# Kernel tuning notes

Hardware: AMD Instinct MI355X
Metric: run time of the kernel (lower is better)

The kernel has to match this reference:

```python
import jax, jax.numpy as jnp
import numpy as np

B, T, S, E, H = 2, 1024, 1024, 1024, 16
D = E // H  # head_dim = 64
SCALING = D ** -0.5


def setup_inputs() -> dict:
    key = jax.random.key(0)
    ks = jax.random.split(key, 14)
    inv = 1.0 / np.sqrt(E)
    inp = {
        "query": jax.random.normal(ks[0], (B, T, E), jnp.float32),
        "key": jax.random.normal(ks[1], (B, S, E), jnp.float32),
        "value": jax.random.normal(ks[2], (B, S, E), jnp.float32),
        "key_padding_mask": jax.random.bernoulli(ks[3], 0.1, (B, S)),
        "attn_bias": jax.random.normal(ks[4], (B * H, T, S), jnp.float32),
        "Wq": jax.random.uniform(ks[5], (E, E), jnp.float32, -inv, inv),
        "bq": jax.random.uniform(ks[6], (E,), jnp.float32, -inv, inv),
        "Wk": jax.random.uniform(ks[7], (E, E), jnp.float32, -inv, inv),
        "bk": jax.random.uniform(ks[8], (E,), jnp.float32, -inv, inv),
        "Wv": jax.random.uniform(ks[9], (E, E), jnp.float32, -inv, inv),
        "bv": jax.random.uniform(ks[10], (E,), jnp.float32, -inv, inv),
        "Wo": jax.random.uniform(ks[11], (E, E), jnp.float32, -inv, inv),
        "bo": jax.random.uniform(ks[12], (E,), jnp.float32, -inv, inv),
    }
    return inp


def reference(query, key, value, key_padding_mask, attn_bias,
              Wq, bq, Wk, bk, Wv, bv, Wo, bo):
    # Projections (torch Linear: x @ W.T + b)
    q = query @ Wq.T + bq  # [B, T, E]
    k = key @ Wk.T + bk    # [B, S, E]
    v = value @ Wv.T + bv  # [B, S, E]
    # Split heads -> [B, H, L, D]
    q = q.reshape(B, T, H, D).transpose(0, 2, 1, 3) * SCALING
    k = k.reshape(B, S, H, D).transpose(0, 2, 1, 3)
    v = v.reshape(B, S, H, D).transpose(0, 2, 1, 3)
    # Scores [B, H, T, S]
    attn_weights = jnp.einsum('bhtd,bhsd->bhts', q, k)
    # key_padding_mask: True means masked -> -inf (applied BEFORE bias add)
    attn_weights = jnp.where(key_padding_mask[:, None, None, :], -jnp.inf, attn_weights)
    # softmax_dropout with additive bias (eval mode: dropout is identity)
    attn_weights = attn_weights + attn_bias.reshape(B, H, T, S)
    attn = jax.nn.softmax(attn_weights, axis=-1)
    o = jnp.einsum('bhts,bhsd->bhtd', attn, v)  # [B, H, T, D]
    o = o.transpose(0, 2, 1, 3).reshape(B, T, E)
    return o @ Wo.T + bo
```

## Files before the change

### kernel.cpp

```cpp
#include <hip/hip_runtime.h>
#include <math.h>
#include <stdint.h>

#define B_ 2
#define T_ 1024
#define S_ 1024
#define E_ 1024
#define H_ 16
#define SCALING_ 0.125f

typedef short bf16x8 __attribute__((ext_vector_type(8)));
typedef float f32x4 __attribute__((ext_vector_type(4)));
typedef unsigned short us8 __attribute__((ext_vector_type(8)));
typedef unsigned short ush;

__device__ __forceinline__ ush f2bf(float x) {
    unsigned int u = __float_as_uint(x);
    return (ush)((u + 0x7fffu + ((u >> 16) & 1u)) >> 16);
}
__device__ __forceinline__ float bf2f(ush h) {
    return __uint_as_float(((unsigned int)h) << 16);
}
__device__ __forceinline__ void split_bf(float x, ush& hh, ush& ll) {
    hh = f2bf(x);
    ll = f2bf(x - bf2f(hh));
}
__device__ __forceinline__ void gl_lds16(const void* g, void* l) {
    __builtin_amdgcn_global_load_lds(
        (const __attribute__((address_space(1))) unsigned int*)g,
        (__attribute__((address_space(3))) unsigned int*)l, 16, 0, 0);
}
template <int CTRL>
__device__ __forceinline__ float dpp_ror(float x) {
    int v = __builtin_amdgcn_update_dpp(0, __float_as_int(x), CTRL, 0xf, 0xf, true);
    return __int_as_float(v);
}
#define FENCE() asm volatile("" ::: "memory")
#define BARRIER() do { FENCE(); __builtin_amdgcn_s_barrier(); FENCE(); } while (0)

__global__ void mask_detect_kernel(const unsigned int* __restrict__ p,
                                   int* __restrict__ mode_out) {
    __shared__ int gt1_s, oddnz_s;
    if (threadIdx.x == 0) { gt1_s = 0; oddnz_s = 0; }
    __syncthreads();
    int gt1 = 0;
    for (int i = threadIdx.x; i < 512; i += 256)
        if (p[i] > 1u) gt1 = 1;
    if (gt1) atomicOr(&gt1_s, 1);
    __syncthreads();
    if (gt1_s == 0) {
        int oddnz = 0;
        for (int i = threadIdx.x; i < 2048; i += 256)
            if ((i & 1) && p[i] != 0u) oddnz = 1;
        if (oddnz) atomicOr(&oddnz_s, 1);
    }
    __syncthreads();
    if (threadIdx.x == 0)
        *mode_out = gt1_s ? 1 : (oddnz_s ? 0 : 2);
}

__global__ void mask_norm_kernel(const void* __restrict__ p,
                                 const int* __restrict__ mode_p,
                                 int* __restrict__ mout) {
    int i = blockIdx.x * 256 + threadIdx.x;
    int mode = *mode_p;
    int v;
    if (mode == 1)      v = (int)((const unsigned char*)p)[i];
    else if (mode == 2) v = ((const int*)p)[2 * i];
    else                v = ((const int*)p)[i];
    mout[i] = v;
}

__global__ __launch_bounds__(256) void conv_split7_kernel(
    const float* __restrict__ Wq, const float* __restrict__ Wk,
    const float* __restrict__ Wv, const float* __restrict__ Wo,
    const float* __restrict__ xq, const float* __restrict__ xk,
    const float* __restrict__ xv,
    ush* __restrict__ Wqh, ush* __restrict__ Wql,
    ush* __restrict__ Wkh, ush* __restrict__ Wkl,
    ush* __restrict__ Wvh, ush* __restrict__ Wvl,
    ush* __restrict__ Woh, ush* __restrict__ Wol,
    ush* __restrict__ xqh, ush* __restrict__ xql,
    ush* __restrict__ xkh, ush* __restrict__ xkl,
    ush* __restrict__ xvh, ush* __restrict__ xvl) {
    int bid = blockIdx.x;
    const float* src; ush* dh; ush* dl; int lb;
    if (bid < 2048) {
        int w = bid >> 9; lb = bid & 511;
        if (w == 0)      { src = Wq; dh = Wqh; dl = Wql; }
        else if (w == 1) { src = Wk; dh = Wkh; dl = Wkl; }
        else if (w == 2) { src = Wv; dh = Wvh; dl = Wvl; }
        else             { src = Wo; dh = Woh; dl = Wol; }
    } else {
        int a = (bid - 2048) >> 10; lb = (bid - 2048) & 1023;
        if (a == 0)      { src = xq; dh = xqh; dl = xql; }
        else if (a == 1) { src = xk; dh = xkh; dl = xkl; }
        else             { src = xv; dh = xvh; dl = xvl; }
    }
    int i = (lb * 256 + threadIdx.x) * 8;
    float4 a4 = *(const float4*)&src[i];
    float4 b4 = *(const float4*)&src[i + 4];
    float v[8] = {a4.x, a4.y, a4.z, a4.w, b4.x, b4.y, b4.z, b4.w};
    us8 vh, vl;
#pragma unroll
    for (int j = 0; j < 8; j++) {
        ush hh, ll;
        split_bf(v[j], hh, ll);
        vh[j] = hh; vl[j] = ll;
    }
    *(us8*)&dh[i] = vh;
    *(us8*)&dl[i] = vl;
}

template <int N, int K, int ROWBIAS, int SPLITOUT>
__device__ __forceinline__ void gemm_body3(
    int bid,
    const ush* __restrict__ Ahg, const ush* __restrict__ Alg,
    const ush* __restrict__ Bhg, const ush* __restrict__ Blg,
    const float* __restrict__ bias,
    ush* __restrict__ outh, ush* __restrict__ outl,
    float* __restrict__ outf, float alpha, ush* lds) {
    const int tid = threadIdx.x;
    const int lane = tid & 63;
    const int wave = tid >> 6;
    const int wm = wave >> 1, wn = wave & 1;
    const int bn = bid % (N / 64);
    const int bm = bid / (N / 64);
    const int m0 = bm * 64, n0 = bn * 64;
    constexpr int NT = K / 32;
    const int row = tid >> 2, oct = tid & 3;
    const int oct2 = oct ^ ((row >> 1) & 3);

    f32x4 acc[2][2];
#pragma unroll
    for (int i = 0; i < 2; i++)
#pragma unroll
        for (int j = 0; j < 2; j++) acc[i][j] = (f32x4){0.f, 0.f, 0.f, 0.f};

    auto stage = [&](int k0, ush* buf) {
        size_t ga = (size_t)(m0 + row) * K + k0 + oct2 * 8;
        gl_lds16(&Ahg[ga], &buf[tid * 8]);
        gl_lds16(&Alg[ga], &buf[2048 + tid * 8]);
        size_t gb = (size_t)(n0 + row) * K + k0 + oct2 * 8;
        gl_lds16(&Bhg[gb], &buf[4096 + tid * 8]);
        gl_lds16(&Blg[gb], &buf[6144 + tid * 8]);
    };

    ush* p0 = lds;
    ush* p1 = lds + 8192;
    ush* p2 = lds + 16384;
    stage(0, p0);
    stage(32, p1);

    for (int t = 0; t < NT; t++) {
        if (t + 1 < NT) asm volatile("s_waitcnt vmcnt(4)" ::: "memory");
        else            asm volatile("s_waitcnt vmcnt(0)" ::: "memory");
        BARRIER();
        if (t + 2 < NT) stage((t + 2) * 32, p2);

        bf16x8 afr[2][2], bfr[2][2];
#pragma unroll
        for (int nj = 0; nj < 2; nj++) {
            int rowB = wn * 32 + nj * 16 + (lane & 15);
            int ch = (lane >> 4) ^ ((rowB >> 1) & 3);
            bfr[nj][0] = *(const bf16x8*)&p0[4096 + rowB * 32 + ch * 8];
            bfr[nj][1] = *(const bf16x8*)&p0[6144 + rowB * 32 + ch * 8];
        }
#pragma unroll
        for (int mi = 0; mi < 2; mi++) {
            int rowA = wm * 32 + mi * 16 + (lane & 15);
            int ch = (lane >> 4) ^ ((rowA >> 1) & 3);
            afr[mi][0] = *(const bf16x8*)&p0[rowA * 32 + ch * 8];
            afr[mi][1] = *(const bf16x8*)&p0[2048 + rowA * 32 + ch * 8];
        }
        __builtin_amdgcn_s_setprio(1);
#pragma unroll
        for (int mi = 0; mi < 2; mi++)
#pragma unroll
            for (int nj = 0; nj < 2; nj++) {
                acc[mi][nj] = __builtin_amdgcn_mfma_f32_16x16x32_bf16(afr[mi][0], bfr[nj][0], acc[mi][nj], 0, 0, 0);
                acc[mi][nj] = __builtin_amdgcn_mfma_f32_16x16x32_bf16(afr[mi][1], bfr[nj][0], acc[mi][nj], 0, 0, 0);
                acc[mi][nj] = __builtin_amdgcn_mfma_f32_16x16x32_bf16(afr[mi][0], bfr[nj][1], acc[mi][nj], 0, 0, 0);
            }
        __builtin_amdgcn_s_setprio(0);

        ush* tmp = p0; p0 = p1; p1 = p2; p2 = tmp;
    }

    float bcol[2];
    if (!ROWBIAS) {
#pragma unroll
        for (int nj = 0; nj < 2; nj++)
            bcol[nj] = bias[n0 + wn * 32 + nj * 16 + (lane & 15)];
    }
#pragma unroll
    for (int mi = 0; mi < 2; mi++) {
#pragma unroll
        for (int r = 0; r < 4; r++) {
            int orow = m0 + wm * 32 + mi * 16 + (lane >> 4) * 4 + r;
            float brow = ROWBIAS ? bias[orow] : 0.f;
#pragma unroll
            for (int nj = 0; nj < 2; nj++) {
                int col = n0 + wn * 32 + nj * 16 + (lane & 15);
                float v = alpha * (acc[mi][nj][r] + (ROWBIAS ? brow : bcol[nj]));
                if (SPLITOUT) {
                    ush hh, ll;
                    split_bf(v, hh, ll);
                    outh[(size_t)orow * N + col] = hh;
                    outl[(size_t)orow * N + col] = ll;
                } else {
                    outf[(size_t)orow * N + col] = v;
                }
            }
        }
    }
}

__global__ __launch_bounds__(256) void proj_fused_kernel(
    const ush* __restrict__ xqh, const ush* __restrict__ xql,
    const ush* __restrict__ xkh, const ush* __restrict__ xkl,
    const ush* __restrict__ xvh, const ush* __restrict__ xvl,
    const ush* __restrict__ Wqh, const ush* __restrict__ Wql,
    const ush* __restrict__ Wkh, const ush* __restrict__ Wkl,
    const ush* __restrict__ Wvh, const ush* __restrict__ Wvl,
    const float* __restrict__ bq, const float* __restrict__ bk,
    const float* __restrict__ bv_,
    ush* __restrict__ qh, ush* __restrict__ ql,
    ush* __restrict__ kh, ush* __restrict__ kl,
    ush* __restrict__ vth, ush* __restrict__ vtl) {
    __shared__ __align__(16) ush lds[3 * 8192];
    int op = blockIdx.x / 512;
    int bid = blockIdx.x % 512;
    if (op == 0)
        gemm_body3<1024, 1024, 0, 1>(bid, xqh, xql, Wqh, Wql, bq,
                                     qh, ql, nullptr, SCALING_, lds);
    else if (op == 1)
        gemm_body3<1024, 1024, 0, 1>(bid, xkh, xkl, Wkh, Wkl, bk,
                                     kh, kl, nullptr, 1.f, lds);
    else
        gemm_body3<2048, 1024, 1, 1>(bid, Wvh, Wvl, xvh, xvl, bv_,
                                     vth, vtl, nullptr, 1.f, lds);
}

__global__ __launch_bounds__(256) void gemm_out_kernel(
    const ush* __restrict__ oh, const ush* __restrict__ ol,
    const ush* __restrict__ Woh, const ush* __restrict__ Wol,
    const float* __restrict__ bo, float* __restrict__ out) {
    __shared__ __align__(16) ush lds[3 * 8192];
    gemm_body3<1024, 1024, 0, 0>(blockIdx.x, oh, ol, Woh, Wol, bo,
                                 nullptr, nullptr, out, 1.f, lds);
}

__global__ __launch_bounds__(256) void flash_kernel(
    const ush* __restrict__ qh, const ush* __restrict__ ql,
    const ush* __restrict__ kh, const ush* __restrict__ kl,
    const ush* __restrict__ vth, const ush* __restrict__ vtl,
    const float* __restrict__ bias, const int* __restrict__ mask,
    ush* __restrict__ oh, ush* __restrict__ ol) {
    __shared__ __align__(16) ush Ksh[2][4096], Ksl[2][4096];
    __shared__ __align__(16) ush Vsh[4096], Vsl[4096];
    __shared__ __align__(16) float BPb[2][4096];

    const int tid = threadIdx.x;
    const int lane = tid & 63;
    const int wave = tid >> 6;
    const int bh = blockIdx.x >> 4;
    const int tt = blockIdx.x & 15;
    const int b = bh >> 4, h = bh & 15;
    const int t0 = tt * 64;
    const int srow = tid >> 3;
    const int soct = tid & 7;

#pragma unroll
    for (int p = 0; p < 2; p++) {
        int row = p * 32 + srow;
        int oc2 = soct ^ (row & 7);
        size_t g = (size_t)(b * T_ + t0 + row) * E_ + h * 64 + oc2 * 8;
        gl_lds16(&qh[g], &Ksh[0][row * 64 + soct * 8]);
        gl_lds16(&ql[g], &Ksl[0][row * 64 + soct * 8]);
    }
    asm volatile("s_waitcnt vmcnt(0)" ::: "memory");
    __syncthreads();
    bf16x8 qfh[2], qfl[2];
    {
        int row = wave * 16 + (lane & 15);
#pragma unroll
        for (int kk = 0; kk < 2; kk++) {
            int ch = (kk * 4 + (lane >> 4)) ^ (row & 7);
            qfh[kk] = *(const bf16x8*)&Ksh[0][row * 64 + ch * 8];
            qfl[kk] = *(const bf16x8*)&Ksl[0][row * 64 + ch * 8];
        }
    }
    __syncthreads();

    float mrow[4] = {-INFINITY, -INFINITY, -INFINITY, -INFINITY};
    float lrow[4] = {0.f, 0.f, 0.f, 0.f};
    f32x4 oacc[4];
#pragma unroll
    for (int dj = 0; dj < 4; dj++) oacc[dj] = (f32x4){0.f, 0.f, 0.f, 0.f};

    auto stage_k = [&](int ti, int c) {
#pragma unroll
        for (int p = 0; p < 2; p++) {
            int row = p * 32 + srow;
            int oc2 = soct ^ (row & 7);
            size_t gk = (size_t)(b * S_ + ti * 64 + row) * E_ + h * 64 + oc2 * 8;
            gl_lds16(&kh[gk], &Ksh[c][row * 64 + soct * 8]);
            gl_lds16(&kl[gk], &Ksl[c][row * 64 + soct * 8]);
        }
    };
    auto stage_v = [&](int ti) {
#pragma unroll
        for (int p = 0; p < 2; p++) {
            int row = p * 32 + srow;
            int oc2 = soct ^ (row & 7);
            size_t gv = (size_t)(h * 64 + row) * (B_ * S_) + b * S_ + ti * 64 + oc2 * 8;
            gl_lds16(&vth[gv], &Vsh[row * 64 + soct * 8]);
            gl_lds16(&vtl[gv], &Vsl[row * 64 + soct * 8]);
        }
    };
    auto stage_bias = [&](int ti, int reg) {
#pragma unroll
        for (int p = 0; p < 4; p++) {
            int row = p * 16 + (tid >> 4);
            int slot = tid & 15;
            int sslot = slot ^ (((row >> 2) & 1) << 2);
            const float* src = bias + ((size_t)bh * T_ + t0 + row) * S_ +
                               ti * 64 + sslot * 4;
            gl_lds16(src, &BPb[reg][(p * 256 + tid) * 4]);
        }
    };

    int mk[4];
    stage_k(0, 0);
    stage_v(0);
    stage_bias(0, 0);
#pragma unroll
    for (int nj = 0; nj < 4; nj++)
        mk[nj] = mask[b * S_ + nj * 16 + (lane & 15)];
    asm volatile("s_waitcnt vmcnt(0)" ::: "memory");
    __syncthreads();

    for (int t = 0; t < 16; t++) {
        const int cur = t & 1;

        if (t < 15) {
            stage_k(t + 1, cur ^ 1);
            stage_bias(t + 1, cur ^ 1);
        }

        f32x4 sc[4];
#pragma unroll
        for (int nj = 0; nj < 4; nj++) sc[nj] = (f32x4){0.f, 0.f, 0.f, 0.f};
        __builtin_amdgcn_s_setprio(1);
#pragma unroll
        for (int kk = 0; kk < 2; kk++) {
#pragma unroll
            for (int nj = 0; nj < 4; nj++) {
                int row = nj * 16 + (lane & 15);
                int ch = (kk * 4 + (lane >> 4)) ^ (row & 7);
                bf16x8 kfh = *(const bf16x8*)&Ksh[cur][row * 64 + ch * 8];
                bf16x8 kfl = *(const bf16x8*)&Ksl[cur][row * 64 + ch * 8];
                sc[nj] = __builtin_amdgcn_mfma_f32_16x16x32_bf16(qfh[kk], kfh, sc[nj], 0, 0, 0);
                sc[nj] = __builtin_amdgcn_mfma_f32_16x16x32_bf16(qfl[kk], kfh, sc[nj], 0, 0, 0);
                sc[nj] = __builtin_amdgcn_mfma_f32_16x16x32_bf16(qfh[kk], kfl, sc[nj], 0, 0, 0);
            }
        }
        __builtin_amdgcn_s_setprio(0);

        {
            const float* bp = &BPb[cur][wave * 1024];
#pragma unroll
            for (int r = 0; r < 4; r++) {
                int tl = (lane >> 4) * 4 + r;
                int sx = ((tl >> 2) & 1) << 4;
#pragma unroll
                for (int nj = 0; nj < 4; nj++) {
                    int s = (nj * 16 + (lane & 15)) ^ sx;
                    float bvv = bp[tl * 64 + s];
                    float v = mk[nj] ? -INFINITY : sc[nj][r];
                    sc[nj][r] = v + bvv;
                }
            }
        }
        if (t < 15) {
            const int s0n = (t + 1) * 64;
#pragma unroll
            for (int nj = 0; nj < 4; nj++)
                mk[nj] = mask[b * S_ + s0n + nj * 16 + (lane & 15)];
        }

        ush phv[4][4], plv[4][4];
#pragma unroll
        for (int r = 0; r < 4; r++) {
            float mx = fmaxf(fmaxf(sc[0][r], sc[1][r]), fmaxf(sc[2][r], sc[3][r]));
            mx = fmaxf(mx, dpp_ror<0x121>(mx));
            mx = fmaxf(mx, dpp_ror<0x122>(mx));
            mx = fmaxf(mx, dpp_ror<0x124>(mx));
            mx = fmaxf(mx, dpp_ror<0x128>(mx));
            float mnew = fmaxf(mrow[r], mx);
            float esc = __expf(mrow[r] - mnew);
            float ps = 0.f;
#pragma unroll
            for (int nj = 0; nj < 4; nj++) {
                float p = __expf(sc[nj][r] - mnew);
                ps += p;
                split_bf(p, phv[nj][r], plv[nj][r]);
            }
            ps += dpp_ror<0x121>(ps);
            ps += dpp_ror<0x122>(ps);
            ps += dpp_ror<0x124>(ps);
            ps += dpp_ror<0x128>(ps);
            lrow[r] = lrow[r] * esc + ps;
            mrow[r] = mnew;
#pragma unroll
            for (int dj = 0; dj < 4; dj++) oacc[dj][r] *= esc;
        }

        ush* Pw = (ush*)&BPb[cur][wave * 1024];
#pragma unroll
        for (int r = 0; r < 4; r++) {
            int tq = (lane >> 4) * 4 + r;
            int f = (((tq >> 2) & 3) << 1) | (tq & 1);
#pragma unroll
            for (int nj = 0; nj < 4; nj++) {
                int s = nj * 16 + (lane & 15);
                int idx = tq * 64 + (((s >> 3) ^ f) * 8) + (s & 7);
                Pw[idx] = phv[nj][r];
                Pw[1024 + idx] = plv[nj][r];
            }
        }
        bf16x8 pah[2], pal[2];
        {
            int tq = lane & 15;
            int f = (((tq >> 2) & 3) << 1) | (tq & 1);
#pragma unroll
            for (int kk = 0; kk < 2; kk++) {
                int ch = (kk * 4 + (lane >> 4)) ^ f;
                pah[kk] = *(const bf16x8*)&Pw[tq * 64 + ch * 8];
                pal[kk] = *(const bf16x8*)&Pw[1024 + tq * 64 + ch * 8];
            }
        }

        if (t < 15) asm volatile("s_waitcnt vmcnt(8)" ::: "memory");
        else        asm volatile("s_waitcnt vmcnt(0)" ::: "memory");

        __builtin_amdgcn_s_setprio(1);
#pragma unroll
        for (int dj = 0; dj < 4; dj++) {
            int row = dj * 16 + (lane & 15);
#pragma unroll
            for (int kk = 0; kk < 2; kk++) {
                int ch = (kk * 4 + (lane >> 4)) ^ (row & 7);
                bf16x8 vfh = *(const bf16x8*)&Vsh[row * 64 + ch * 8];
                bf16x8 vfl = *(const bf16x8*)&Vsl[row * 64 + ch * 8];
                oacc[dj] = __builtin_amdgcn_mfma_f32_16x16x32_bf16(pah[kk], vfh, oacc[dj], 0, 0, 0);
                oacc[dj] = __builtin_amdgcn_mfma_f32_16x16x32_bf16(pal[kk], vfh, oacc[dj], 0, 0, 0);
                oacc[dj] = __builtin_amdgcn_mfma_f32_16x16x32_bf16(pah[kk], vfl, oacc[dj], 0, 0, 0);
            }
        }
        __builtin_amdgcn_s_setprio(0);

        asm volatile("s_waitcnt vmcnt(0)" ::: "memory");
        BARRIER();
        if (t < 15) stage_v(t + 1);
    }

#pragma unroll
    for (int r = 0; r < 4; r++) {
        float inv = 1.f / lrow[r];
        int t = t0 + wave * 16 + (lane >> 4) * 4 + r;
#pragma unroll
        for (int dj = 0; dj < 4; dj++) {
            float v = oacc[dj][r] * inv;
            ush hh, ll;
            split_bf(v, hh, ll);
            size_t g = (size_t)(b * T_ + t) * E_ + h * 64 + dj * 16 + (lane & 15);
            oh[g] = hh;
            ol[g] = ll;
        }
    }
}

extern "C" void kernel_launch(void* const* d_in, const int* in_sizes, int n_in,
                              void* d_out, int out_size, void* d_ws,
                              size_t ws_size, hipStream_t stream) {
    const float* query = (const float*)d_in[0];
    const float* key   = (const float*)d_in[1];
    const float* value = (const float*)d_in[2];
    const void*  kpm   = d_in[3];
    const float* attn_bias = (const float*)d_in[4];
    const float* Wq = (const float*)d_in[5];
    const float* bq = (const float*)d_in[6];
    const float* Wk = (const float*)d_in[7];
    const float* bk = (const float*)d_in[8];
    const float* Wv = (const float*)d_in[9];
    const float* bv = (const float*)d_in[10];
    const float* Wo = (const float*)d_in[11];
    const float* bo = (const float*)d_in[12];
    float* out = (float*)d_out;

    char* ws = (char*)d_ws;
    const size_t MB = 1024 * 1024;
    ush* Wqh = (ush*)(ws + 0 * MB);
    ush* Wql = (ush*)(ws + 2 * MB);
    ush* Wkh = (ush*)(ws + 4 * MB);
    ush* Wkl = (ush*)(ws + 6 * MB);
    ush* Wvh = (ush*)(ws + 8 * MB);
    ush* Wvl = (ush*)(ws + 10 * MB);
    ush* Woh = (ush*)(ws + 12 * MB);
    ush* Wol = (ush*)(ws + 14 * MB);
    ush* qh  = (ush*)(ws + 16 * MB);
    ush* ql  = (ush*)(ws + 20 * MB);
    ush* kh  = (ush*)(ws + 24 * MB);
    ush* kl  = (ush*)(ws + 28 * MB);
    ush* vth = (ush*)(ws + 32 * MB);
    ush* vtl = (ush*)(ws + 36 * MB);
    ush* xqh = (ush*)(ws + 40 * MB);
    ush* xql = (ush*)(ws + 44 * MB);
    ush* xkh = (ush*)(ws + 48 * MB);
    ush* xkl = (ush*)(ws + 52 * MB);
    ush* xvh = (ush*)(ws + 56 * MB);
    ush* xvl = (ush*)(ws + 60 * MB);
    ush* oh  = (ush*)(ws + 40 * MB);
    ush* ol  = (ush*)(ws + 44 * MB);
    int* masknorm = (int*)(ws + 64 * MB);
    int* mode = masknorm + 2048;

    conv_split7_kernel<<<5120, 256, 0, stream>>>(
        Wq, Wk, Wv, Wo, query, key, value,
        Wqh, Wql, Wkh, Wkl, Wvh, Wvl, Woh, Wol,
        xqh, xql, xkh, xkl, xvh, xvl);
    mask_detect_kernel<<<1, 256, 0, stream>>>((const unsigned int*)kpm, mode);
    mask_norm_kernel<<<8, 256, 0, stream>>>(kpm, mode, masknorm);

    proj_fused_kernel<<<1536, 256, 0, stream>>>(
        xqh, xql, xkh, xkl, xvh, xvl,
        Wqh, Wql, Wkh, Wkl, Wvh, Wvl, bq, bk, bv,
        qh, ql, kh, kl, vth, vtl);

    flash_kernel<<<512, 256, 0, stream>>>(qh, ql, kh, kl, vth, vtl, attn_bias,
                                          masknorm, oh, ol);

    gemm_out_kernel<<<512, 256, 0, stream>>>(oh, ol, Woh, Wol, bo, out);
}
```

Baseline: 344.9 us.

## Load attention bias directly into registers and reuse K buffer for P staging

Attention bias is no longer staged through a shared-memory double buffer. Each lane now loads its bias values and mask straight from global memory into ping-pong register arrays, one tile ahead. The P tile staging moves into the current K buffer slot, which frees the bias LDS space and should raise occupancy. The vmcnt waits and barriers are reordered to fit the new load counts. The trade-off is more registers, scalar (non-vectorized) global bias loads, and fragile hand-counted vmcnt values.

```diff
diff --git a/kernel.cpp b/kernel.cpp
--- a/kernel.cpp
+++ b/kernel.cpp
@@ -259,14 +259,13 @@
     ush* __restrict__ oh, ush* __restrict__ ol) {
     __shared__ __align__(16) ush Ksh[2][4096], Ksl[2][4096];
     __shared__ __align__(16) ush Vsh[4096], Vsl[4096];
-    __shared__ __align__(16) float BPb[2][4096];
 
     const int tid = threadIdx.x;
     const int lane = tid & 63;
     const int wave = tid >> 6;
-    const int bh = blockIdx.x >> 4;
+    const int bhid = blockIdx.x >> 4;
     const int tt = blockIdx.x & 15;
-    const int b = bh >> 4, h = bh & 15;
+    const int b = bhid >> 4, h = bhid & 15;
     const int t0 = tt * 64;
     const int srow = tid >> 3;
     const int soct = tid & 7;
@@ -299,6 +298,8 @@
 #pragma unroll
     for (int dj = 0; dj < 4; dj++) oacc[dj] = (f32x4){0.f, 0.f, 0.f, 0.f};
 
+    const size_t bias0 = ((size_t)bhid * T_ + t0 + wave * 16) * S_;
+
     auto stage_k = [&](int ti, int c) {
 #pragma unroll
         for (int p = 0; p < 2; p++) {
@@ -319,34 +320,39 @@
             gl_lds16(&vtl[gv], &Vsl[row * 64 + soct * 8]);
         }
     };
-    auto stage_bias = [&](int ti, int reg) {
-#pragma unroll
-        for (int p = 0; p < 4; p++) {
-            int row = p * 16 + (tid >> 4);
-            int slot = tid & 15;
-            int sslot = slot ^ (((row >> 2) & 1) << 2);
-            const float* src = bias + ((size_t)bh * T_ + t0 + row) * S_ +
-                               ti * 64 + sslot * 4;
-            gl_lds16(src, &BPb[reg][(p * 256 + tid) * 4]);
-        }
-    };
-
-    int mk[4];
+
+    float bvA[4][4], bvB[4][4];
+    int mkA[4], mkB[4];
+
     stage_k(0, 0);
     stage_v(0);
-    stage_bias(0, 0);
-#pragma unroll
-    for (int nj = 0; nj < 4; nj++)
-        mk[nj] = mask[b * S_ + nj * 16 + (lane & 15)];
+    FENCE();
+#pragma unroll
+    for (int nj = 0; nj < 4; nj++) {
+        int s = nj * 16 + (lane & 15);
+        mkA[nj] = mask[b * S_ + s];
+#pragma unroll
+        for (int r = 0; r < 4; r++)
+            bvA[nj][r] = bias[bias0 + (size_t)((lane >> 4) * 4 + r) * S_ + s];
+    }
     asm volatile("s_waitcnt vmcnt(0)" ::: "memory");
     __syncthreads();
 
-    for (int t = 0; t < 16; t++) {
-        const int cur = t & 1;
-
+    auto iter = [&](int t, int cur, float (&bvU)[4][4], float (&bvL)[4][4],
+                    int (&mkU)[4], int (&mkL)[4]) {
         if (t < 15) {
             stage_k(t + 1, cur ^ 1);
-            stage_bias(t + 1, cur ^ 1);
+            FENCE();
+            const int s0n = (t + 1) * 64;
+#pragma unroll
+            for (int nj = 0; nj < 4; nj++) {
+                int s = s0n + nj * 16 + (lane & 15);
+                mkL[nj] = mask[b * S_ + s];
+#pragma unroll
+                for (int r = 0; r < 4; r++)
+                    bvL[nj][r] = bias[bias0 + (size_t)((lane >> 4) * 4 + r) * S_ + s];
+            }
+            FENCE();
         }
 
         f32x4 sc[4];
@@ -368,29 +374,18 @@
         }
         __builtin_amdgcn_s_setprio(0);
 
-        {
-            const float* bp = &BPb[cur][wave * 1024];
+        if (t < 15) asm volatile("s_waitcnt vmcnt(24)" ::: "memory");
+        else        asm volatile("s_waitcnt vmcnt(0)" ::: "memory");
+        BARRIER();
+
+        ush phv[4][4], plv[4][4];
+#pragma unroll
+        for (int nj = 0; nj < 4; nj++)
 #pragma unroll
             for (int r = 0; r < 4; r++) {
-                int tl = (lane >> 4) * 4 + r;
-                int sx = ((tl >> 2) & 1) << 4;
-#pragma unroll
-                for (int nj = 0; nj < 4; nj++) {
-                    int s = (nj * 16 + (lane & 15)) ^ sx;
-                    float bvv = bp[tl * 64 + s];
-                    float v = mk[nj] ? -INFINITY : sc[nj][r];
-                    sc[nj][r] = v + bvv;
-                }
-            }
-        }
-        if (t < 15) {
-            const int s0n = (t + 1) * 64;
-#pragma unroll
-            for (int nj = 0; nj < 4; nj++)
-                mk[nj] = mask[b * S_ + s0n + nj * 16 + (lane & 15)];
-        }
-
-        ush phv[4][4], plv[4][4];
+                float v = mkU[nj] ? -INFINITY : sc[nj][r];
+                sc[nj][r] = v + bvU[nj][r];
+            }
 #pragma unroll
         for (int r = 0; r < 4; r++) {
             float mx = fmaxf(fmaxf(sc[0][r], sc[1][r]), fmaxf(sc[2][r], sc[3][r]));
@@ -417,7 +412,8 @@
             for (int dj = 0; dj < 4; dj++) oacc[dj][r] *= esc;
         }
 
-        ush* Pw = (ush*)&BPb[cur][wave * 1024];
+        ush* Pwh = &Ksh[cur][wave * 1024];
+        ush* Pwl = &Ksl[cur][wave * 1024];
 #pragma unroll
         for (int r = 0; r < 4; r++) {
             int tq = (lane >> 4) * 4 + r;
@@ -426,8 +422,8 @@
             for (int nj = 0; nj < 4; nj++) {
                 int s = nj * 16 + (lane & 15);
                 int idx = tq * 64 + (((s >> 3) ^ f) * 8) + (s & 7);
-                Pw[idx] = phv[nj][r];
-                Pw[1024 + idx] = plv[nj][r];
+                Pwh[idx] = phv[nj][r];
+                Pwl[idx] = plv[nj][r];
             }
         }
         bf16x8 pah[2], pal[2];
@@ -437,13 +433,10 @@
 #pragma unroll
             for (int kk = 0; kk < 2; kk++) {
                 int ch = (kk * 4 + (lane >> 4)) ^ f;
-                pah[kk] = *(const bf16x8*)&Pw[tq * 64 + ch * 8];
-                pal[kk] = *(const bf16x8*)&Pw[1024 + tq * 64 + ch * 8];
-            }
-        }
-
-        if (t < 15) asm volatile("s_waitcnt vmcnt(8)" ::: "memory");
-        else        asm volatile("s_waitcnt vmcnt(0)" ::: "memory");
+                pah[kk] = *(const bf16x8*)&Pwh[tq * 64 + ch * 8];
+                pal[kk] = *(const bf16x8*)&Pwl[tq * 64 + ch * 8];
+            }
+        }
 
         __builtin_amdgcn_s_setprio(1);
 #pragma unroll
@@ -461,9 +454,15 @@
         }
         __builtin_amdgcn_s_setprio(0);
 
-        asm volatile("s_waitcnt vmcnt(0)" ::: "memory");
+        if (t < 15) asm volatile("s_waitcnt vmcnt(20)" ::: "memory");
+        else        asm volatile("s_waitcnt vmcnt(0)" ::: "memory");
         BARRIER();
-        if (t < 15) stage_v(t + 1);
+        if (t < 15) { stage_v(t + 1); FENCE(); }
+    };
+
+    for (int tp = 0; tp < 8; tp++) {
+        iter(2 * tp,     0, bvA, bvB, mkA, mkB);
+        iter(2 * tp + 1, 1, bvB, bvA, mkB, mkA);
     }
 
 #pragma unroll
```

After: 350.2 us. Within noise of the previous version (+1.5%).
